# Kernel tuning notes

Hardware: AMD Instinct MI355X
Metric: run time of the kernel (lower is better)

Reference implementation:

```python
import jax, jax.numpy as jnp
import numpy as np

B, D, N, MSRC, H = 4, 256, 2048, 2048, 4
DIM = D // H  # per-head dim = 64
EPS = 1e-3


def _conv1x1(W, b, z):
    # 1x1 Conv1d == per-position linear: W [out,in], z [B,in,N]
    return jnp.einsum('oc,bcn->bon', W, z) + b[None, :, None]


def setup_inputs() -> dict:
    key = jax.random.key(0)
    ks = jax.random.split(key, 20)
    s = 0.05
    x = jax.random.normal(ks[0], (B, D, N), dtype=jnp.float32)
    source = jax.random.normal(ks[1], (B, D, MSRC), dtype=jnp.float32)
    mask = (jax.random.uniform(ks[2], (B, N, MSRC)) > 0.3).astype(jnp.float32)
    Wq = jax.random.normal(ks[3], (D, D), jnp.float32) * s
    bq = jax.random.normal(ks[4], (D,), jnp.float32) * s
    Wk = jax.random.normal(ks[5], (D, D), jnp.float32) * s
    bk = jax.random.normal(ks[6], (D,), jnp.float32) * s
    Wv = jax.random.normal(ks[7], (D, D), jnp.float32) * s
    bv = jax.random.normal(ks[8], (D,), jnp.float32) * s
    Wm = jax.random.normal(ks[9], (D, D), jnp.float32) * s
    bm = jax.random.normal(ks[10], (D,), jnp.float32) * s
    W1 = jax.random.normal(ks[11], (2 * D, 2 * D), jnp.float32) * s
    b1 = jax.random.normal(ks[12], (2 * D,), jnp.float32) * s
    gamma = jnp.ones((2 * D,), jnp.float32)
    beta = jnp.zeros((2 * D,), jnp.float32)
    rmean = jax.random.normal(ks[13], (2 * D,), jnp.float32) * 0.1
    rvar = jax.random.uniform(ks[14], (2 * D,), jnp.float32) + 0.5
    W2 = jax.random.normal(ks[15], (D, 2 * D), jnp.float32) * s
    b2 = jnp.zeros((D,), jnp.float32)  # nn.init.constant_(mlp[-1].bias, 0.0)
    return dict(x=x, source=source, mask=mask, Wq=Wq, bq=bq, Wk=Wk, bk=bk,
                Wv=Wv, bv=bv, Wm=Wm, bm=bm, W1=W1, b1=b1, gamma=gamma,
                beta=beta, rmean=rmean, rvar=rvar, W2=W2, b2=b2)


def reference(x, source, mask, Wq, bq, Wk, bk, Wv, bv, Wm, bm,
              W1, b1, gamma, beta, rmean, rvar, W2, b2):
    b = x.shape[0]
    # channel dim split as (dim, heads) per torch .view(B, dim, H, -1)
    q = _conv1x1(Wq, bq, x).reshape(b, DIM, H, -1)        # [B,d,H,N]
    k = _conv1x1(Wk, bk, source).reshape(b, DIM, H, -1)   # [B,d,H,M]
    v = _conv1x1(Wv, bv, source).reshape(b, DIM, H, -1)   # [B,d,H,M]
    scores = jnp.einsum('bdhn,bdhm->bhnm', q, k) / (DIM ** 0.5)
    neg = -jnp.finfo(scores.dtype).max
    scores = jnp.where(mask[:, None, :, :] > 0, scores, neg)
    prob = jax.nn.softmax(scores, axis=-1)                # [B,H,N,M]
    msg = jnp.einsum('bhnm,bdhm->bdhn', prob, v).reshape(b, D, -1)
    message = _conv1x1(Wm, bm, msg)                       # [B,D,N]
    y = jnp.concatenate([x, message], axis=1)             # [B,2D,N]
    h = _conv1x1(W1, b1, y)
    # BatchNorm1d (eval mode, eps=1e-3)
    h = (h - rmean[None, :, None]) * jax.lax.rsqrt(rvar + EPS)[None, :, None]
    h = h * gamma[None, :, None] + beta[None, :, None]
    h = jax.nn.relu(h)
    return _conv1x1(W2, b2, h)                            # [B,D,N]
```

## Files before the change

kernel.cpp:

```cpp
#include <hip/hip_runtime.h>

constexpr int Bb = 4;
constexpr int Dd = 256;
constexpr int Nn = 2048;
constexpr int Mm = 2048;
constexpr int Hh = 4;
constexpr int D2 = 512;
constexpr int NT = Bb * Nn;

#define FMAXV 3.402823466e38f

typedef _Float16 half8 __attribute__((ext_vector_type(8)));
typedef _Float16 half4v __attribute__((ext_vector_type(4)));
typedef float f32x4 __attribute__((ext_vector_type(4)));

__global__ __launch_bounds__(256)
void prep_weights_kernel(const float* __restrict__ Wq, const float* __restrict__ bq,
                         const float* __restrict__ Wk, const float* __restrict__ bk,
                         const float* __restrict__ Wv, const float* __restrict__ bv,
                         const float* __restrict__ Wm,
                         const float* __restrict__ W1, const float* __restrict__ b1,
                         const float* __restrict__ gamma, const float* __restrict__ beta,
                         const float* __restrict__ rmean, const float* __restrict__ rvar,
                         const float* __restrict__ W2, const float* __restrict__ mask,
                         _Float16* __restrict__ Wqp, float* __restrict__ bqp,
                         _Float16* __restrict__ Wkvp, float* __restrict__ bkvp,
                         _Float16* __restrict__ Wmp,
                         _Float16* __restrict__ W1p, float* __restrict__ b1f,
                         _Float16* __restrict__ W2p,
                         unsigned long long* __restrict__ bmask) {
    const int r = blockIdx.x, t = threadIdx.x;
    if (r < 256) {
        const int h = r >> 6, d = r & 63, so = d * Hh + h;
        Wqp[r * 256 + t] = (_Float16)Wq[so * 256 + t];
        if (t == 0) bqp[r] = bq[so];
    } else if (r < 768) {
        const int rr = r - 256, part = rr >> 8, o = rr & 255;
        const int h = o >> 6, d = o & 63, so = d * Hh + h;
        const float* Ws = part ? Wv : Wk;
        const float* bs = part ? bv : bk;
        Wkvp[rr * 256 + t] = (_Float16)Ws[so * 256 + t];
        if (t == 0) bkvp[rr] = bs[so];
    } else if (r < 1024) {
        const int o = r - 768;
        const int h = t >> 6, d = t & 63, sk = d * Hh + h;
        Wmp[o * 256 + t] = (_Float16)Wm[o * 256 + sk];
    } else if (r < 1536) {
        const int o = r - 1024;
        const float s = gamma[o] * rsqrtf(rvar[o] + 1e-3f);
        W1p[o * 512 + t]       = (_Float16)(W1[o * 512 + t] * s);
        W1p[o * 512 + t + 256] = (_Float16)(W1[o * 512 + t + 256] * s);
        if (t == 0) b1f[o] = (b1[o] - rmean[o]) * s + beta[o];
    } else if (r < 1792) {
        const int o = r - 1536;
        W2p[o * 512 + t]       = (_Float16)W2[o * 512 + t];
        W2p[o * 512 + t + 256] = (_Float16)W2[o * 512 + t + 256];
    } else {
        const int id = r - 1792;
        const int w = t >> 6, lane = t & 63;
        const int row = id * 4 + w;
        const float* mrow = mask + (size_t)row * Mm;
        unsigned long long* brow = bmask + (size_t)row * (Mm / 64);
        #pragma unroll 4
        for (int word = 0; word < Mm / 64; ++word) {
            const float v = mrow[word * 64 + lane];
            const unsigned long long bits = __ballot(v > 0.f);
            if (lane == 0) brow[word] = bits;
        }
    }
}

__global__ __launch_bounds__(256)
void prep_x_kernel(const float* __restrict__ x, const float* __restrict__ source,
                   _Float16* __restrict__ Yp, _Float16* __restrict__ Sp) {
    __shared__ _Float16 Ts[64][72];
    const int z = blockIdx.z, b = z >> 1, which = z & 1;
    const float* src = which ? source : x;
    _Float16* dst = which ? Sp : Yp;
    const int stride = which ? 256 : 512;
    const int c0 = blockIdx.y * 64, n0 = blockIdx.x * 64;
    const int t = threadIdx.x;
    const int cl = t >> 2, np = (t & 3) * 16;
    const float* sp = src + ((size_t)b * Dd + c0 + cl) * Nn + n0 + np;
    #pragma unroll
    for (int i = 0; i < 4; ++i) {
        float4 v = *(const float4*)(sp + i * 4);
        Ts[np + i * 4 + 0][cl] = (_Float16)v.x;
        Ts[np + i * 4 + 1][cl] = (_Float16)v.y;
        Ts[np + i * 4 + 2][cl] = (_Float16)v.z;
        Ts[np + i * 4 + 3][cl] = (_Float16)v.w;
    }
    __syncthreads();
    const int nl = t >> 2, cp = (t & 3) * 16;
    half8 a0 = *(const half8*)&Ts[nl][cp];
    half8 a1 = *(const half8*)&Ts[nl][cp + 8];
    _Float16* dp = dst + ((size_t)b * Nn + n0 + nl) * stride + c0 + cp;
    *(half8*)dp = a0;
    *(half8*)(dp + 8) = a1;
}

__global__ __launch_bounds__(64)
void gemm16_kernel(const _Float16* __restrict__ A, const _Float16* __restrict__ A2,
                   const _Float16* __restrict__ W, const float* __restrict__ bias,
                   _Float16* __restrict__ dst0, _Float16* __restrict__ dst1,
                   _Float16* __restrict__ dst2, float* __restrict__ dstF,
                   int K, int sA, int sOut, int modeSel, int relu) {
    __shared__ _Float16 Es[16][72];
    const int lane = threadIdx.x & 63, quad = lane >> 4, l16 = lane & 15;
    const int n0 = blockIdx.x * 64;
    const int og0 = blockIdx.y * 64;

    int mode = 0, oloc0 = og0;
    const _Float16* Ab = A;
    int sAl = sA;
    _Float16* d0 = dst0;
    if (modeSel == 3) {
        if (blockIdx.y >= 4) {
            Ab = A2; sAl = 256;
            if (blockIdx.y < 8) { d0 = dst1; oloc0 = og0 - 256; }
            else { mode = 1; oloc0 = og0 - 512; }
        }
    } else if (modeSel == 2) {
        mode = 2;
    }

    const _Float16* aRow[4];
    const _Float16* bRow[4];
    #pragma unroll
    for (int i = 0; i < 4; ++i)
        aRow[i] = Ab + (size_t)(n0 + i * 16 + l16) * sAl + quad * 8;
    #pragma unroll
    for (int j = 0; j < 4; ++j)
        bRow[j] = W + (size_t)(og0 + j * 16 + l16) * K + quad * 8;

    f32x4 acc[4][4] = {};
    half8 a0[4], b0[4], a1[4], b1[4];
    #pragma unroll
    for (int i = 0; i < 4; ++i) a0[i] = *(const half8*)(aRow[i]);
    #pragma unroll
    for (int j = 0; j < 4; ++j) b0[j] = *(const half8*)(bRow[j]);

    #pragma unroll 1
    for (int k0 = 0; k0 < K; k0 += 64) {
        #pragma unroll
        for (int i = 0; i < 4; ++i) a1[i] = *(const half8*)(aRow[i] + k0 + 32);
        #pragma unroll
        for (int j = 0; j < 4; ++j) b1[j] = *(const half8*)(bRow[j] + k0 + 32);
        #pragma unroll
        for (int i = 0; i < 4; ++i)
            #pragma unroll
            for (int j = 0; j < 4; ++j)
                acc[i][j] = __builtin_amdgcn_mfma_f32_16x16x32_f16(a0[i], b0[j], acc[i][j], 0, 0, 0);
        if (k0 + 64 < K) {
            #pragma unroll
            for (int i = 0; i < 4; ++i) a0[i] = *(const half8*)(aRow[i] + k0 + 64);
            #pragma unroll
            for (int j = 0; j < 4; ++j) b0[j] = *(const half8*)(bRow[j] + k0 + 64);
        }
        #pragma unroll
        for (int i = 0; i < 4; ++i)
            #pragma unroll
            for (int j = 0; j < 4; ++j)
                acc[i][j] = __builtin_amdgcn_mfma_f32_16x16x32_f16(a1[i], b1[j], acc[i][j], 0, 0, 0);
    }

    float bcol[4];
    #pragma unroll
    for (int j = 0; j < 4; ++j) bcol[j] = bias[og0 + j * 16 + l16];

    if (mode == 0) {
        #pragma unroll
        for (int i = 0; i < 4; ++i) {
            #pragma unroll
            for (int j = 0; j < 4; ++j)
                #pragma unroll
                for (int reg = 0; reg < 4; ++reg) {
                    float v = acc[i][j][reg] + bcol[j];
                    if (relu) v = fmaxf(v, 0.f);
                    Es[quad * 4 + reg][j * 16 + l16] = (_Float16)v;
                }
            __asm__ volatile("s_waitcnt lgkmcnt(0)" ::: "memory");
            const int row = lane & 15, oseg = (lane >> 4) * 16;
            half8 e0 = *(const half8*)&Es[row][oseg];
            half8 e1 = *(const half8*)&Es[row][oseg + 8];
            _Float16* dp = d0 + (size_t)(n0 + i * 16 + row) * sOut + oloc0 + oseg;
            *(half8*)dp = e0;
            *(half8*)(dp + 8) = e1;
            __asm__ volatile("s_waitcnt lgkmcnt(0)" ::: "memory");
        }
    } else if (mode == 1) {
        #pragma unroll
        for (int i = 0; i < 4; ++i) {
            const int ng = n0 + i * 16 + quad * 4;
            const int bidx = ng >> 11, m0 = ng & 2047;
            #pragma unroll
            for (int j = 0; j < 4; ++j) {
                const int o = oloc0 + j * 16 + l16;
                half4v pv;
                #pragma unroll
                for (int reg = 0; reg < 4; ++reg) pv[reg] = (_Float16)(acc[i][j][reg] + bcol[j]);
                *(half4v*)(dst2 + ((size_t)bidx * 256 + o) * (size_t)Mm + m0) = pv;
            }
        }
    } else {
        #pragma unroll
        for (int i = 0; i < 4; ++i) {
            const int ng = n0 + i * 16 + quad * 4;
            const int bidx = ng >> 11, m0 = ng & 2047;
            #pragma unroll
            for (int j = 0; j < 4; ++j) {
                const int o = og0 + j * 16 + l16;
                f32x4 v;
                #pragma unroll
                for (int reg = 0; reg < 4; ++reg) v[reg] = acc[i][j][reg] + bcol[j];
                *(f32x4*)(dstF + ((size_t)bidx * 256 + o) * (size_t)Nn + m0) = v;
            }
        }
    }
}

__global__ __launch_bounds__(256)
void attn_mfma_kernel(const _Float16* __restrict__ Qp, const _Float16* __restrict__ Kp,
                      const _Float16* __restrict__ Vt,
                      const unsigned int* __restrict__ bmask,
                      _Float16* __restrict__ msgp) {
    __shared__ __align__(16) _Float16 Ks[2][64][72];
    __shared__ __align__(16) _Float16 Vs[2][64][72];
    __shared__ __align__(16) _Float16 Ps[4][16][72];

    const int b = blockIdx.z, h = blockIdx.y, n0 = blockIdx.x * 64;
    const int t = threadIdx.x;
    const int w = t >> 6, lane = t & 63, quad = lane >> 4, l16 = lane & 15;

    const _Float16* qp = Qp + ((size_t)b * Nn + n0 + w * 16 + l16) * 256 + h * 64 + quad * 8;
    const half8 qa0 = *(const half8*)(qp);
    const half8 qa1 = *(const half8*)(qp + 32);

    const _Float16* Kstg = Kp + (size_t)b * Nn * 256 + h * 64;
    const _Float16* Vstg = Vt + ((size_t)b * 256 + h * 64) * (size_t)Mm;
    const int sr = t >> 2, sc = (t & 3) * 16;

    const unsigned int* bmBase = bmask + ((size_t)b * Nn + n0 + w * 16 + quad * 4) * (Mm / 32);

    float lo[4] = {0.f, 0.f, 0.f, 0.f};
    f32x4 O[4] = {};

    half8 sk0, sk1, sv0, sv1;
    auto stage_load = [&](int m0) {
        const _Float16* ks = Kstg + (size_t)(m0 + sr) * 256 + sc;
        sk0 = *(const half8*)(ks);
        sk1 = *(const half8*)(ks + 8);
        const _Float16* vs = Vstg + (size_t)sr * Mm + m0 + sc;
        sv0 = *(const half8*)(vs);
        sv1 = *(const half8*)(vs + 8);
    };
    auto stage_write = [&](int buf) {
        *(half8*)&Ks[buf][sr][sc]     = sk0;
        *(half8*)&Ks[buf][sr][sc + 8] = sk1;
        *(half8*)&Vs[buf][sr][sc]     = sv0;
        *(half8*)&Vs[buf][sr][sc + 8] = sv1;
    };

    stage_load(0);
    stage_write(0);
    __syncthreads();

    #pragma unroll 1
    for (int it = 0; it < Mm / 64; ++it) {
        const int m0 = it * 64, cur = it & 1;
        if (it < Mm / 64 - 1) stage_load(m0 + 64);

        uint2 bmv[4];
        #pragma unroll
        for (int reg = 0; reg < 4; ++reg)
            bmv[reg] = *(const uint2*)(bmBase + (size_t)reg * (Mm / 32) + (m0 >> 5));

        f32x4 S[4];
        #pragma unroll
        for (int mt = 0; mt < 4; ++mt) {
            half8 k0 = *(const half8*)&Ks[cur][mt * 16 + l16][quad * 8];
            half8 k1 = *(const half8*)&Ks[cur][mt * 16 + l16][32 + quad * 8];
            f32x4 z = {0.f, 0.f, 0.f, 0.f};
            z = __builtin_amdgcn_mfma_f32_16x16x32_f16(qa0, k0, z, 0, 0, 0);
            z = __builtin_amdgcn_mfma_f32_16x16x32_f16(qa1, k1, z, 0, 0, 0);
            S[mt] = z;
        }

        float p[4][4];
        #pragma unroll
        for (int reg = 0; reg < 4; ++reg) {
            const unsigned losh = bmv[reg].x >> l16;
            const unsigned hish = bmv[reg].y >> l16;
            p[0][reg] = (losh & 1u)         ? __expf(S[0][reg] * 0.125f) : 0.f;
            p[1][reg] = ((losh >> 16) & 1u) ? __expf(S[1][reg] * 0.125f) : 0.f;
            p[2][reg] = (hish & 1u)         ? __expf(S[2][reg] * 0.125f) : 0.f;
            p[3][reg] = ((hish >> 16) & 1u) ? __expf(S[3][reg] * 0.125f) : 0.f;
        }
        #pragma unroll
        for (int reg = 0; reg < 4; ++reg)
            lo[reg] += (p[0][reg] + p[1][reg]) + (p[2][reg] + p[3][reg]);

        #pragma unroll
        for (int mt = 0; mt < 4; ++mt)
            #pragma unroll
            for (int reg = 0; reg < 4; ++reg)
                Ps[w][quad * 4 + reg][mt * 16 + l16] = (_Float16)p[mt][reg];
        __asm__ volatile("s_waitcnt lgkmcnt(0)" ::: "memory");
        half8 pa0 = *(const half8*)&Ps[w][l16][quad * 8];
        half8 pa1 = *(const half8*)&Ps[w][l16][32 + quad * 8];

        #pragma unroll
        for (int dt = 0; dt < 4; ++dt) {
            half8 v0 = *(const half8*)&Vs[cur][dt * 16 + l16][quad * 8];
            half8 v1 = *(const half8*)&Vs[cur][dt * 16 + l16][32 + quad * 8];
            O[dt] = __builtin_amdgcn_mfma_f32_16x16x32_f16(pa0, v0, O[dt], 0, 0, 0);
            O[dt] = __builtin_amdgcn_mfma_f32_16x16x32_f16(pa1, v1, O[dt], 0, 0, 0);
        }

        if (it < Mm / 64 - 1) stage_write(cur ^ 1);
        __syncthreads();
    }

    #pragma unroll
    for (int reg = 0; reg < 4; ++reg) {
        float s = lo[reg];
        s += __shfl_xor(s, 1);
        s += __shfl_xor(s, 2);
        s += __shfl_xor(s, 4);
        s += __shfl_xor(s, 8);
        lo[reg] = 1.0f / s;
    }

    _Float16* op = msgp + ((size_t)b * Nn + n0 + w * 16 + quad * 4) * 256 + h * 64 + l16;
    #pragma unroll
    for (int reg = 0; reg < 4; ++reg)
        #pragma unroll
        for (int dt = 0; dt < 4; ++dt)
            op[(size_t)reg * 256 + dt * 16] = (_Float16)(O[dt][reg] * lo[reg]);
}

extern "C" void kernel_launch(void* const* d_in, const int* in_sizes, int n_in,
                              void* d_out, int out_size, void* d_ws, size_t ws_size,
                              hipStream_t stream) {
    const float* x      = (const float*)d_in[0];
    const float* source = (const float*)d_in[1];
    const float* mask   = (const float*)d_in[2];
    const float* Wq = (const float*)d_in[3];
    const float* bq = (const float*)d_in[4];
    const float* Wk = (const float*)d_in[5];
    const float* bk = (const float*)d_in[6];
    const float* Wv = (const float*)d_in[7];
    const float* bv = (const float*)d_in[8];
    const float* Wm = (const float*)d_in[9];
    const float* bm = (const float*)d_in[10];
    const float* W1 = (const float*)d_in[11];
    const float* b1 = (const float*)d_in[12];
    const float* gamma = (const float*)d_in[13];
    const float* beta  = (const float*)d_in[14];
    const float* rmean = (const float*)d_in[15];
    const float* rvar  = (const float*)d_in[16];
    const float* W2 = (const float*)d_in[17];
    const float* b2 = (const float*)d_in[18];
    float* outp = (float*)d_out;

    char* wsb = (char*)d_ws;
    _Float16* Yp   = (_Float16*)wsb;
    _Float16* Sp   = (_Float16*)(wsb + (8u << 20));
    _Float16* Qp   = (_Float16*)(wsb + (12u << 20));
    _Float16* Kp   = (_Float16*)(wsb + (16u << 20));
    _Float16* Vt   = (_Float16*)(wsb + (20u << 20));
    _Float16* msgp = (_Float16*)(wsb + (24u << 20));
    _Float16* Hp   = (_Float16*)(wsb + (28u << 20));
    unsigned long long* bmask = (unsigned long long*)(wsb + (28u << 20));
    char* wp = wsb + (36u << 20);
    _Float16* Wqp  = (_Float16*)wp;            wp += 256 * 256 * 2;
    _Float16* Wkvp = (_Float16*)wp;            wp += 512 * 256 * 2;
    _Float16* Wmp  = (_Float16*)wp;            wp += 256 * 256 * 2;
    _Float16* W1p  = (_Float16*)wp;            wp += 512 * 512 * 2;
    _Float16* W2p  = (_Float16*)wp;            wp += 256 * 512 * 2;
    float* bqp  = (float*)wp;                  wp += 256 * 4;
    float* bkvp = (float*)wp;                  wp += 512 * 4;
    float* b1f  = (float*)wp;                  wp += 512 * 4;

    prep_weights_kernel<<<3840, 256, 0, stream>>>(
        Wq, bq, Wk, bk, Wv, bv, Wm, W1, b1, gamma, beta, rmean, rvar, W2, mask,
        Wqp, bqp, Wkvp, bkvp, Wmp, W1p, b1f, W2p, bmask);

    dim3 gPrep(Nn / 64, Dd / 64, Bb * 2);
    prep_x_kernel<<<gPrep, 256, 0, stream>>>(x, source, Yp, Sp);

    gemm16_kernel<<<dim3(NT / 64, 12), 64, 0, stream>>>(
        Yp, Sp, Wqp, bqp, Qp, Kp, Vt, nullptr, 256, 512, 256, 3, 0);

    dim3 gAttn(Nn / 64, Hh, Bb);
    attn_mfma_kernel<<<gAttn, 256, 0, stream>>>(Qp, Kp, Vt,
                                                (const unsigned int*)bmask, msgp);

    gemm16_kernel<<<dim3(NT / 64, 4), 64, 0, stream>>>(
        msgp, nullptr, Wmp, bm, Yp + 256, nullptr, nullptr, nullptr, 256, 256, 512, 0, 0);
    gemm16_kernel<<<dim3(NT / 64, 8), 64, 0, stream>>>(
        Yp, nullptr, W1p, b1f, Hp, nullptr, nullptr, nullptr, 512, 512, 512, 0, 1);
    gemm16_kernel<<<dim3(NT / 64, 4), 64, 0, stream>>>(
        Hp, nullptr, W2p, b2, nullptr, nullptr, nullptr, outp, 512, 512, 0, 2, 0);
}
```

Measured before the change: 272.4 us.

## Rewrite projection GEMMs as 4-wave 128x128 tiles with async LDS double-buffering

The single-wave 64x64 GEMM kernel that read operands straight from global memory is replaced by a 256-thread kernel computing 128x128 tiles. Each of its four waves owns a 64x64 sub-tile, and operands are staged into XOR-swizzled shared memory with global_load_lds, double-buffered across K steps. The aim is more operand reuse per global byte and more latency hiding across the four projection/MLP GEMMs. In exchange there are fewer blocks (lower grid parallelism), extra barriers, and a larger shared-memory footprint per block.

```diff
diff --git a/kernel.cpp b/kernel.cpp
--- a/kernel.cpp
+++ b/kernel.cpp
@@ -13,6 +13,13 @@
 typedef _Float16 half8 __attribute__((ext_vector_type(8)));
 typedef _Float16 half4v __attribute__((ext_vector_type(4)));
 typedef float f32x4 __attribute__((ext_vector_type(4)));
+
+typedef const __attribute__((address_space(1))) void* gas_p;
+typedef __attribute__((address_space(3))) void* las_p;
+
+__device__ __forceinline__ void gload16(const void* g, void* l) {
+    __builtin_amdgcn_global_load_lds((gas_p)g, (las_p)l, 16, 0, 0);
+}
 
 __global__ __launch_bounds__(256)
 void prep_weights_kernel(const float* __restrict__ Wq, const float* __restrict__ bq,
@@ -99,74 +106,94 @@
     *(half8*)(dp + 8) = a1;
 }
 
-__global__ __launch_bounds__(64)
-void gemm16_kernel(const _Float16* __restrict__ A, const _Float16* __restrict__ A2,
+__global__ __launch_bounds__(256)
+void gemm4w_kernel(const _Float16* __restrict__ A, const _Float16* __restrict__ A2,
                    const _Float16* __restrict__ W, const float* __restrict__ bias,
                    _Float16* __restrict__ dst0, _Float16* __restrict__ dst1,
                    _Float16* __restrict__ dst2, float* __restrict__ dstF,
                    int K, int sA, int sOut, int modeSel, int relu) {
-    __shared__ _Float16 Es[16][72];
-    const int lane = threadIdx.x & 63, quad = lane >> 4, l16 = lane & 15;
-    const int n0 = blockIdx.x * 64;
-    const int og0 = blockIdx.y * 64;
+    __shared__ __align__(16) _Float16 As[2][128][64];
+    __shared__ __align__(16) _Float16 Bs[2][128][64];
+    __shared__ __align__(16) _Float16 Es[4][16][72];
+
+    const int t = threadIdx.x;
+    const int w = t >> 6, lane = t & 63, quad = lane >> 4, l16 = lane & 15;
+    const int wr = w >> 1, wc = w & 1;
+    const int n0 = blockIdx.x * 128;
+    const int og0 = blockIdx.y * 128;
 
     int mode = 0, oloc0 = og0;
     const _Float16* Ab = A;
     int sAl = sA;
     _Float16* d0 = dst0;
     if (modeSel == 3) {
-        if (blockIdx.y >= 4) {
-            Ab = A2; sAl = 256;
-            if (blockIdx.y < 8) { d0 = dst1; oloc0 = og0 - 256; }
-            else { mode = 1; oloc0 = og0 - 512; }
-        }
+        const int part = blockIdx.y >> 1;
+        if (part == 1)      { Ab = A2; sAl = 256; d0 = dst1; oloc0 = og0 - 256; }
+        else if (part == 2) { Ab = A2; sAl = 256; mode = 1; oloc0 = og0 - 512; }
     } else if (modeSel == 2) {
         mode = 2;
     }
 
-    const _Float16* aRow[4];
-    const _Float16* bRow[4];
-    #pragma unroll
-    for (int i = 0; i < 4; ++i)
-        aRow[i] = Ab + (size_t)(n0 + i * 16 + l16) * sAl + quad * 8;
-    #pragma unroll
-    for (int j = 0; j < 4; ++j)
-        bRow[j] = W + (size_t)(og0 + j * 16 + l16) * K + quad * 8;
+    const int srow = t >> 3, sslot = t & 7;
+    const int schunk = sslot ^ (srow & 7);
 
     f32x4 acc[4][4] = {};
-    half8 a0[4], b0[4], a1[4], b1[4];
-    #pragma unroll
-    for (int i = 0; i < 4; ++i) a0[i] = *(const half8*)(aRow[i]);
-    #pragma unroll
-    for (int j = 0; j < 4; ++j) b0[j] = *(const half8*)(bRow[j]);
+
+    const int nk = K / 64;
+    int buf = 0;
+
+    {
+        #pragma unroll
+        for (int c = 0; c < 4; ++c) {
+            const int row = c * 32 + srow;
+            gload16(Ab + (size_t)(n0 + row) * sAl + schunk * 8,
+                    (_Float16*)As + c * 2048 + t * 8);
+            gload16(W + (size_t)(og0 + row) * K + schunk * 8,
+                    (_Float16*)Bs + c * 2048 + t * 8);
+        }
+        __asm__ volatile("s_waitcnt vmcnt(0)" ::: "memory");
+        __syncthreads();
+    }
 
     #pragma unroll 1
-    for (int k0 = 0; k0 < K; k0 += 64) {
-        #pragma unroll
-        for (int i = 0; i < 4; ++i) a1[i] = *(const half8*)(aRow[i] + k0 + 32);
-        #pragma unroll
-        for (int j = 0; j < 4; ++j) b1[j] = *(const half8*)(bRow[j] + k0 + 32);
-        #pragma unroll
-        for (int i = 0; i < 4; ++i)
+    for (int kt = 0; kt < nk; ++kt) {
+        if (kt + 1 < nk) {
+            const int k0 = (kt + 1) * 64, nb = buf ^ 1;
+            #pragma unroll
+            for (int c = 0; c < 4; ++c) {
+                const int row = c * 32 + srow;
+                gload16(Ab + (size_t)(n0 + row) * sAl + k0 + schunk * 8,
+                        (_Float16*)As + nb * 8192 + c * 2048 + t * 8);
+                gload16(W + (size_t)(og0 + row) * K + k0 + schunk * 8,
+                        (_Float16*)Bs + nb * 8192 + c * 2048 + t * 8);
+            }
+        }
+        #pragma unroll
+        for (int ks = 0; ks < 2; ++ks) {
+            const int csw = ((ks * 4 + quad) ^ (l16 & 7)) * 8;
+            half8 af[4], bf[4];
+            #pragma unroll
+            for (int i = 0; i < 4; ++i)
+                af[i] = *(const half8*)&As[buf][wr * 64 + i * 16 + l16][csw];
             #pragma unroll
             for (int j = 0; j < 4; ++j)
-                acc[i][j] = __builtin_amdgcn_mfma_f32_16x16x32_f16(a0[i], b0[j], acc[i][j], 0, 0, 0);
-        if (k0 + 64 < K) {
-            #pragma unroll
-            for (int i = 0; i < 4; ++i) a0[i] = *(const half8*)(aRow[i] + k0 + 64);
-            #pragma unroll
-            for (int j = 0; j < 4; ++j) b0[j] = *(const half8*)(bRow[j] + k0 + 64);
-        }
-        #pragma unroll
-        for (int i = 0; i < 4; ++i)
-            #pragma unroll
-            for (int j = 0; j < 4; ++j)
-                acc[i][j] = __builtin_amdgcn_mfma_f32_16x16x32_f16(a1[i], b1[j], acc[i][j], 0, 0, 0);
+                bf[j] = *(const half8*)&Bs[buf][wc * 64 + j * 16 + l16][csw];
+            #pragma unroll
+            for (int i = 0; i < 4; ++i)
+                #pragma unroll
+                for (int j = 0; j < 4; ++j)
+                    acc[i][j] = __builtin_amdgcn_mfma_f32_16x16x32_f16(af[i], bf[j], acc[i][j], 0, 0, 0);
+        }
+        if (kt + 1 < nk) {
+            __asm__ volatile("s_waitcnt vmcnt(0)" ::: "memory");
+            __syncthreads();
+            buf ^= 1;
+        }
     }
 
     float bcol[4];
     #pragma unroll
-    for (int j = 0; j < 4; ++j) bcol[j] = bias[og0 + j * 16 + l16];
+    for (int j = 0; j < 4; ++j) bcol[j] = bias[og0 + wc * 64 + j * 16 + l16];
 
     if (mode == 0) {
         #pragma unroll
@@ -177,13 +204,14 @@
                 for (int reg = 0; reg < 4; ++reg) {
                     float v = acc[i][j][reg] + bcol[j];
                     if (relu) v = fmaxf(v, 0.f);
-                    Es[quad * 4 + reg][j * 16 + l16] = (_Float16)v;
+                    Es[w][quad * 4 + reg][j * 16 + l16] = (_Float16)v;
                 }
             __asm__ volatile("s_waitcnt lgkmcnt(0)" ::: "memory");
             const int row = lane & 15, oseg = (lane >> 4) * 16;
-            half8 e0 = *(const half8*)&Es[row][oseg];
-            half8 e1 = *(const half8*)&Es[row][oseg + 8];
-            _Float16* dp = d0 + (size_t)(n0 + i * 16 + row) * sOut + oloc0 + oseg;
+            half8 e0 = *(const half8*)&Es[w][row][oseg];
+            half8 e1 = *(const half8*)&Es[w][row][oseg + 8];
+            _Float16* dp = d0 + (size_t)(n0 + wr * 64 + i * 16 + row) * sOut
+                         + oloc0 + wc * 64 + oseg;
             *(half8*)dp = e0;
             *(half8*)(dp + 8) = e1;
             __asm__ volatile("s_waitcnt lgkmcnt(0)" ::: "memory");
@@ -191,11 +219,11 @@
     } else if (mode == 1) {
         #pragma unroll
         for (int i = 0; i < 4; ++i) {
-            const int ng = n0 + i * 16 + quad * 4;
+            const int ng = n0 + wr * 64 + i * 16 + quad * 4;
             const int bidx = ng >> 11, m0 = ng & 2047;
             #pragma unroll
             for (int j = 0; j < 4; ++j) {
-                const int o = oloc0 + j * 16 + l16;
+                const int o = oloc0 + wc * 64 + j * 16 + l16;
                 half4v pv;
                 #pragma unroll
                 for (int reg = 0; reg < 4; ++reg) pv[reg] = (_Float16)(acc[i][j][reg] + bcol[j]);
@@ -205,11 +233,11 @@
     } else {
         #pragma unroll
         for (int i = 0; i < 4; ++i) {
-            const int ng = n0 + i * 16 + quad * 4;
+            const int ng = n0 + wr * 64 + i * 16 + quad * 4;
             const int bidx = ng >> 11, m0 = ng & 2047;
             #pragma unroll
             for (int j = 0; j < 4; ++j) {
-                const int o = og0 + j * 16 + l16;
+                const int o = og0 + wc * 64 + j * 16 + l16;
                 f32x4 v;
                 #pragma unroll
                 for (int reg = 0; reg < 4; ++reg) v[reg] = acc[i][j][reg] + bcol[j];
@@ -389,17 +417,17 @@
     dim3 gPrep(Nn / 64, Dd / 64, Bb * 2);
     prep_x_kernel<<<gPrep, 256, 0, stream>>>(x, source, Yp, Sp);
 
-    gemm16_kernel<<<dim3(NT / 64, 12), 64, 0, stream>>>(
+    gemm4w_kernel<<<dim3(NT / 128, 6), 256, 0, stream>>>(
         Yp, Sp, Wqp, bqp, Qp, Kp, Vt, nullptr, 256, 512, 256, 3, 0);
 
     dim3 gAttn(Nn / 64, Hh, Bb);
     attn_mfma_kernel<<<gAttn, 256, 0, stream>>>(Qp, Kp, Vt,
                                                 (const unsigned int*)bmask, msgp);
 
-    gemm16_kernel<<<dim3(NT / 64, 4), 64, 0, stream>>>(
+    gemm4w_kernel<<<dim3(NT / 128, 2), 256, 0, stream>>>(
         msgp, nullptr, Wmp, bm, Yp + 256, nullptr, nullptr, nullptr, 256, 256, 512, 0, 0);
-    gemm16_kernel<<<dim3(NT / 64, 8), 64, 0, stream>>>(
+    gemm4w_kernel<<<dim3(NT / 128, 4), 256, 0, stream>>>(
         Yp, nullptr, W1p, b1f, Hp, nullptr, nullptr, nullptr, 512, 512, 512, 0, 1);
-    gemm16_kernel<<<dim3(NT / 64, 4), 64, 0, stream>>>(
+    gemm4w_kernel<<<dim3(NT / 128, 2), 256, 0, stream>>>(
         Hp, nullptr, W2p, b2, nullptr, nullptr, nullptr, outp, 512, 512, 0, 2, 0);
 }
```

Result: faster. 248.8 us (-8.6%).
